# Kernel optimization log

Measured on AMD Instinct MI355X. Metric: run time of the kernel, lower is better.

## Reference

```python
import jax, jax.numpy as jnp
import numpy as np
from jax import lax

WIN_SIZE = 11
SIGMA = 1.5
K1, K2 = 0.01, 0.03
DATA_RANGE = 1.0


def _gauss_1d(size=WIN_SIZE, sigma=SIGMA):
    coords = jnp.arange(size, dtype=jnp.float32) - size // 2
    g = jnp.exp(-(coords ** 2) / (2.0 * sigma ** 2))
    return g / jnp.sum(g)


def _blur(x, win):
    # x: (1, C, H, W); separable depthwise gaussian, VALID padding (pytorch_msssim)
    C = x.shape[1]
    dn = ('NCHW', 'OIHW', 'NCHW')
    kw = jnp.tile(win.reshape(1, 1, 1, -1), (C, 1, 1, 1))  # (C,1,1,K)
    kh = jnp.tile(win.reshape(1, 1, -1, 1), (C, 1, 1, 1))  # (C,1,K,1)
    x = lax.conv_general_dilated(x, kw, (1, 1), 'VALID',
                                 dimension_numbers=dn, feature_group_count=C)
    x = lax.conv_general_dilated(x, kh, (1, 1), 'VALID',
                                 dimension_numbers=dn, feature_group_count=C)
    return x


def _ssim_loss(pred, targ, height, width):
    x = pred.reshape(1, 3, height, width)
    y = targ.reshape(1, 3, height, width)
    win = _gauss_1d()
    C1 = (K1 * DATA_RANGE) ** 2
    C2 = (K2 * DATA_RANGE) ** 2

    mu1 = _blur(x, win)
    mu2 = _blur(y, win)
    mu1_sq = mu1 * mu1
    mu2_sq = mu2 * mu2
    mu1_mu2 = mu1 * mu2
    sigma1_sq = _blur(x * x, win) - mu1_sq
    sigma2_sq = _blur(y * y, win) - mu2_sq
    sigma12 = _blur(x * y, win) - mu1_mu2

    cs_map = (2.0 * sigma12 + C2) / (sigma1_sq + sigma2_sq + C2)
    ssim_map = ((2.0 * mu1_mu2 + C1) / (mu1_sq + mu2_sq + C1)) * cs_map
    return 1.0 - jnp.mean(ssim_map)


def setup_inputs() -> dict:
    key = jax.random.key(0)
    k1, k2 = jax.random.split(key)
    H, W = 2048, 2048
    return {
        'predicted_img': jax.random.uniform(k1, (1, 3, H, W), dtype=jnp.float32),
        'target_img': jax.random.uniform(k2, (1, 3, H, W), dtype=jnp.float32),
        'height': H,
        'width': W,
    }


def reference(predicted_img, target_img, height, width):
    return _ssim_loss(predicted_img, target_img, height, width)
```

## Files before the change

### kernel.cpp

```cpp
#include <hip/hip_runtime.h>
#include <math.h>

typedef float f32x2 __attribute__((ext_vector_type(2)));
typedef float f32x4 __attribute__((ext_vector_type(4)));

#define HH    2048
#define WW    2048
#define NCH   3
#define NOUT  2038
#define OWID  64
#define OH    128
#define CROWS 8
#define BUF   20
#define HAW   66
#define HCW   68
#define NTX   32
#define NTY   16
#define NBLOCKS (NTX*NTY*NCH)
#define NOUT_TOTAL 12460332.0f

__device__ __forceinline__ float ssim_term(float mu1, float mu2,
                                           float b11, float b22, float b12) {
    const float c1v = 1e-4f, c2v = 9e-4f;
    float mu1sq = mu1 * mu1;
    float mu2sq = mu2 * mu2;
    float mu12  = mu1 * mu2;
    float s11 = b11 - mu1sq;
    float s22 = b22 - mu2sq;
    float s12 = b12 - mu12;
    float csn = 2.f * s12 + c2v;
    float csd = s11 + s22 + c2v;
    float ln  = 2.f * mu12 + c1v;
    float ld  = mu1sq + mu2sq + c1v;
    return (csn * ln) * __builtin_amdgcn_rcpf(csd * ld);
}

__global__ __launch_bounds__(256, 2)
void ssim_main(const float* __restrict__ x, const float* __restrict__ y,
               float* __restrict__ partials) {
    __shared__ f32x2 hbA[BUF][HAW];
    __shared__ f32x2 hbB[BUF][HAW];
    __shared__ float hbC[BUF][HCW];
    __shared__ float wsum[4];

    const int tid = threadIdx.x;
    const int gx0 = blockIdx.x * OWID;
    const int gy0 = blockIdx.y * OH;
    const float* xb = x + (size_t)blockIdx.z * HH * WW;
    const float* yb = y + (size_t)blockIdx.z * HH * WW;

    float w[11];
    {
        float s = 0.f;
        #pragma unroll
        for (int i = 0; i < 11; ++i) {
            float d = (float)(i - 5);
            w[i] = expf(-d * d / 4.5f);
            s += w[i];
        }
        float inv = 1.f / s;
        #pragma unroll
        for (int i = 0; i < 11; ++i) w[i] *= inv;
    }

    const int lr  = tid >> 5;
    const int c0  = (tid & 31) * 2;
    const int gxc = gx0 + c0;

    f32x4 px[3], py[3];

    auto PF = [&](int base) {
        int gy = gy0 + base + lr; if (gy > HH - 1) gy = HH - 1;
        const float* xr = xb + (size_t)gy * WW;
        const float* yr = yb + (size_t)gy * WW;
        #pragma unroll
        for (int a = 0; a < 3; ++a) {
            int g = gxc + 4 * a;
            if (g + 4 <= WW) {
                px[a] = *(const f32x4*)(xr + g);
                py[a] = *(const f32x4*)(yr + g);
            } else {
                int g0 = g     < WW ? g     : WW - 1;
                int g1 = g + 1 < WW ? g + 1 : WW - 1;
                int g2 = g + 2 < WW ? g + 2 : WW - 1;
                int g3 = g + 3 < WW ? g + 3 : WW - 1;
                px[a] = (f32x4){xr[g0], xr[g1], xr[g2], xr[g3]};
                py[a] = (f32x4){yr[g0], yr[g1], yr[g2], yr[g3]};
            }
        }
    };

    auto BLUR = [&](int base, bool tailMask) {
        int slot = (base + lr) % BUF;
        f32x2 p[12];
        #pragma unroll
        for (int a = 0; a < 3; ++a)
            #pragma unroll
            for (int i = 0; i < 4; ++i)
                p[4 * a + i] = (f32x2){px[a][i], py[a][i]};
        f32x2 q[12]; float pr[12];
        #pragma unroll
        for (int t = 0; t < 12; ++t) {
            q[t]  = p[t] * p[t];
            pr[t] = p[t].x * p[t].y;
        }
        f32x2 hA[2] = {}, hB[2] = {};
        float hC[2] = {};
        #pragma unroll
        for (int k = 0; k < 11; ++k) {
            f32x2 wk2 = (f32x2){w[k], w[k]};
            #pragma unroll
            for (int j = 0; j < 2; ++j) {
                hA[j] = __builtin_elementwise_fma(wk2, p[j + k], hA[j]);
                hB[j] = __builtin_elementwise_fma(wk2, q[j + k], hB[j]);
                hC[j] = fmaf(w[k], pr[j + k], hC[j]);
            }
        }
        if (!tailMask || lr < 2) {
            *(f32x4*)&hbA[slot][c0] = (f32x4){hA[0].x, hA[0].y, hA[1].x, hA[1].y};
            *(f32x4*)&hbB[slot][c0] = (f32x4){hB[0].x, hB[0].y, hB[1].x, hB[1].y};
            *(f32x2*)&hbC[slot][c0] = (f32x2){hC[0], hC[1]};
        }
    };

    float partial = 0.f;

    PF(0);  BLUR(0, false);
    PF(8);  BLUR(8, false);
    PF(16); BLUR(16, true);
    __syncthreads();

    const int col  = tid & 63;
    const int wid  = tid >> 6;
    const int ocol = gx0 + col;

    for (int m = 0; m < 16; ++m) {
        if (m < 15) PF(8 * m + 18);
        {
            const int r0 = 8 * m + wid * 2;
            int s = r0 % BUF;
            f32x2 aA[2] = {}, aB[2] = {};
            float aC[2] = {};
            #pragma unroll
            for (int j = 0; j < 12; ++j) {
                f32x2 va = hbA[s][col];
                f32x2 vb = hbB[s][col];
                float vc = hbC[s][col];
                #pragma unroll
                for (int i = 0; i < 2; ++i) {
                    const int k = j - i;
                    if (k >= 0 && k < 11) {
                        f32x2 wk2 = (f32x2){w[k], w[k]};
                        aA[i] = __builtin_elementwise_fma(wk2, va, aA[i]);
                        aB[i] = __builtin_elementwise_fma(wk2, vb, aB[i]);
                        aC[i] = fmaf(w[k], vc, aC[i]);
                    }
                }
                s = (s == BUF - 1) ? 0 : s + 1;
            }
            #pragma unroll
            for (int i = 0; i < 2; ++i) {
                int orow = gy0 + r0 + i;
                if (orow < NOUT && ocol < NOUT)
                    partial += ssim_term(aA[i].x, aA[i].y, aB[i].x, aB[i].y, aC[i]);
            }
        }
        __syncthreads();
        if (m < 15) {
            BLUR(8 * m + 18, false);
            __syncthreads();
        }
    }

    #pragma unroll
    for (int off = 32; off > 0; off >>= 1)
        partial += __shfl_down(partial, off, 64);
    if ((tid & 63) == 0) wsum[tid >> 6] = partial;
    __syncthreads();
    if (tid == 0) {
        int bid = (blockIdx.z * gridDim.y + blockIdx.y) * gridDim.x + blockIdx.x;
        partials[bid] = wsum[0] + wsum[1] + wsum[2] + wsum[3];
    }
}

__global__ __launch_bounds__(256)
void ssim_finalize(const float* __restrict__ partials, float* __restrict__ out) {
    __shared__ float ws[4];
    float s = 0.f;
    for (int i = threadIdx.x; i < NBLOCKS / 4; i += 256) {
        float4 v = ((const float4*)partials)[i];
        s += (v.x + v.y) + (v.z + v.w);
    }
    #pragma unroll
    for (int off = 32; off > 0; off >>= 1)
        s += __shfl_down(s, off, 64);
    if ((threadIdx.x & 63) == 0) ws[threadIdx.x >> 6] = s;
    __syncthreads();
    if (threadIdx.x == 0)
        out[0] = 1.f - (ws[0] + ws[1] + ws[2] + ws[3]) / NOUT_TOTAL;
}

extern "C" void kernel_launch(void* const* d_in, const int* in_sizes, int n_in,
                              void* d_out, int out_size, void* d_ws, size_t ws_size,
                              hipStream_t stream) {
    const float* x = (const float*)d_in[0];
    const float* y = (const float*)d_in[1];
    float* out = (float*)d_out;
    float* partials = (float*)d_ws;

    dim3 grid(NTX, NTY, NCH);
    ssim_main<<<grid, dim3(256), 0, stream>>>(x, y, partials);
    ssim_finalize<<<1, 256, 0, stream>>>(partials, out);
}
```

Before: 189.3 us.

## Stream rows per column-thread with register rotating vertical blur accumulators

Replaces the tiled two-pass shared-memory scheme with a streaming design. Each thread owns one output column and walks down a 45-row segment. The horizontal blur uses a small per-wave double-buffered LDS stage, and the vertical blur goes into 11 rotating register accumulators. This removes block-wide barriers and the large LDS ring buffer. In exchange it recomputes 10 halo rows per segment, uses many more registers, and issues scalar 4-byte global loads instead of vector loads.

```diff
diff --git a/kernel.cpp b/kernel.cpp
--- a/kernel.cpp
+++ b/kernel.cpp
@@ -2,21 +2,15 @@
 #include <math.h>
 
 typedef float f32x2 __attribute__((ext_vector_type(2)));
-typedef float f32x4 __attribute__((ext_vector_type(4)));
 
 #define HH    2048
 #define WW    2048
 #define NCH   3
 #define NOUT  2038
-#define OWID  64
-#define OH    128
-#define CROWS 8
-#define BUF   20
-#define HAW   66
-#define HCW   68
-#define NTX   32
-#define NTY   16
-#define NBLOCKS (NTX*NTY*NCH)
+#define SH    45
+#define NSEG  46
+#define NBX   8
+#define NBLOCKS (NBX*NSEG*NCH)
 #define NOUT_TOTAL 12460332.0f
 
 __device__ __forceinline__ float ssim_term(float mu1, float mu2,
@@ -38,138 +32,117 @@
 __global__ __launch_bounds__(256, 2)
 void ssim_main(const float* __restrict__ x, const float* __restrict__ y,
                float* __restrict__ partials) {
-    __shared__ f32x2 hbA[BUF][HAW];
-    __shared__ f32x2 hbB[BUF][HAW];
-    __shared__ float hbC[BUF][HCW];
+    __shared__ f32x2 stage[2][4][80];
     __shared__ float wsum[4];
 
-    const int tid = threadIdx.x;
-    const int gx0 = blockIdx.x * OWID;
-    const int gy0 = blockIdx.y * OH;
+    const int tid  = threadIdx.x;
+    const int lane = tid & 63;
+    const int wid  = tid >> 6;
+    const int col  = blockIdx.x * 256 + tid;
+    const int r0   = blockIdx.y * SH;
     const float* xb = x + (size_t)blockIdx.z * HH * WW;
     const float* yb = y + (size_t)blockIdx.z * HH * WW;
 
-    float w[11];
+    f32x2 w2[11];
     {
+        float wtmp[11];
         float s = 0.f;
         #pragma unroll
         for (int i = 0; i < 11; ++i) {
             float d = (float)(i - 5);
-            w[i] = expf(-d * d / 4.5f);
-            s += w[i];
+            wtmp[i] = expf(-d * d / 4.5f);
+            s += wtmp[i];
         }
         float inv = 1.f / s;
         #pragma unroll
-        for (int i = 0; i < 11; ++i) w[i] *= inv;
+        for (int i = 0; i < 11; ++i) w2[i] = (f32x2){wtmp[i] * inv, wtmp[i] * inv};
     }
 
-    const int lr  = tid >> 5;
-    const int c0  = (tid & 31) * 2;
-    const int gxc = gx0 + c0;
+    const int  cB    = (col + 64 < HH) ? col + 64 : HH - 1;
+    const bool colok = col < NOUT;
+    const bool tail  = lane < 16;
 
-    f32x4 px[3], py[3];
-
-    auto PF = [&](int base) {
-        int gy = gy0 + base + lr; if (gy > HH - 1) gy = HH - 1;
-        const float* xr = xb + (size_t)gy * WW;
-        const float* yr = yb + (size_t)gy * WW;
-        #pragma unroll
-        for (int a = 0; a < 3; ++a) {
-            int g = gxc + 4 * a;
-            if (g + 4 <= WW) {
-                px[a] = *(const f32x4*)(xr + g);
-                py[a] = *(const f32x4*)(yr + g);
-            } else {
-                int g0 = g     < WW ? g     : WW - 1;
-                int g1 = g + 1 < WW ? g + 1 : WW - 1;
-                int g2 = g + 2 < WW ? g + 2 : WW - 1;
-                int g3 = g + 3 < WW ? g + 3 : WW - 1;
-                px[a] = (f32x4){xr[g0], xr[g1], xr[g2], xr[g3]};
-                py[a] = (f32x4){yr[g0], yr[g1], yr[g2], yr[g3]};
-            }
-        }
-    };
-
-    auto BLUR = [&](int base, bool tailMask) {
-        int slot = (base + lr) % BUF;
-        f32x2 p[12];
-        #pragma unroll
-        for (int a = 0; a < 3; ++a)
-            #pragma unroll
-            for (int i = 0; i < 4; ++i)
-                p[4 * a + i] = (f32x2){px[a][i], py[a][i]};
-        f32x2 q[12]; float pr[12];
-        #pragma unroll
-        for (int t = 0; t < 12; ++t) {
-            q[t]  = p[t] * p[t];
-            pr[t] = p[t].x * p[t].y;
-        }
-        f32x2 hA[2] = {}, hB[2] = {};
-        float hC[2] = {};
-        #pragma unroll
-        for (int k = 0; k < 11; ++k) {
-            f32x2 wk2 = (f32x2){w[k], w[k]};
-            #pragma unroll
-            for (int j = 0; j < 2; ++j) {
-                hA[j] = __builtin_elementwise_fma(wk2, p[j + k], hA[j]);
-                hB[j] = __builtin_elementwise_fma(wk2, q[j + k], hB[j]);
-                hC[j] = fmaf(w[k], pr[j + k], hC[j]);
-            }
-        }
-        if (!tailMask || lr < 2) {
-            *(f32x4*)&hbA[slot][c0] = (f32x4){hA[0].x, hA[0].y, hA[1].x, hA[1].y};
-            *(f32x4*)&hbB[slot][c0] = (f32x4){hB[0].x, hB[0].y, hB[1].x, hB[1].y};
-            *(f32x2*)&hbC[slot][c0] = (f32x2){hC[0], hC[1]};
-        }
-    };
+    f32x2 accA[11], accB[11];
+    float accC[11];
+    #pragma unroll
+    for (int i = 0; i < 11; ++i) {
+        accA[i] = (f32x2){0.f, 0.f};
+        accB[i] = (f32x2){0.f, 0.f};
+        accC[i] = 0.f;
+    }
 
     float partial = 0.f;
 
-    PF(0);  BLUR(0, false);
-    PF(8);  BLUR(8, false);
-    PF(16); BLUR(16, true);
-    __syncthreads();
+    float cx0, cy0, cx1, cy1;
+    {
+        const float* xr = xb + (size_t)r0 * WW;
+        const float* yr = yb + (size_t)r0 * WW;
+        cx0 = xr[col]; cy0 = yr[col];
+        cx1 = xr[cB];  cy1 = yr[cB];
+    }
 
-    const int col  = tid & 63;
-    const int wid  = tid >> 6;
-    const int ocol = gx0 + col;
+#define PHASE(VB, PH, EMIT) do {                                               \
+    const int vrow = (VB) + (PH);                                              \
+    \
+    int nrow = r0 + vrow + 1; nrow = nrow < HH ? nrow : HH - 1;                \
+    const float* xr = xb + (size_t)nrow * WW;                                  \
+    const float* yr = yb + (size_t)nrow * WW;                                  \
+    float nx0 = xr[col], ny0 = yr[col];                                        \
+    float nx1 = xr[cB],  ny1 = yr[cB];                                         \
+             \
+    f32x2* sb = &stage[vrow & 1][wid][0];                                      \
+    sb[lane] = (f32x2){cx0, cy0};                                              \
+    if (tail) sb[64 + lane] = (f32x2){cx1, cy1};                               \
+            \
+    f32x2 p[11];                                                               \
+    _Pragma("unroll")                                                          \
+    for (int j = 0; j < 11; ++j) p[j] = sb[lane + j];                          \
+                                    \
+    f32x2 hA = w2[0] * p[0];                                                   \
+    f32x2 hB = w2[0] * (p[0] * p[0]);                                          \
+    float hC = w2[0].x * (p[0].x * p[0].y);                                    \
+    _Pragma("unroll")                                                          \
+    for (int k = 1; k < 11; ++k) {                                             \
+        hA = __builtin_elementwise_fma(w2[k], p[k], hA);                       \
+        hB = __builtin_elementwise_fma(w2[k], p[k] * p[k], hB);                \
+        hC = fmaf(w2[k].x, p[k].x * p[k].y, hC);                               \
+    }                                                                          \
+     \
+     \
+     \
+    accA[(PH)] = w2[0] * hA;                                                   \
+    accB[(PH)] = w2[0] * hB;                                                   \
+    accC[(PH)] = w2[0].x * hC;                                                 \
+    _Pragma("unroll")                                                          \
+    for (int k = 1; k < 11; ++k) {                                             \
+        const int sidx = ((PH) + 11 - k) % 11;                                 \
+        accA[sidx] = __builtin_elementwise_fma(w2[k], hA, accA[sidx]);         \
+        accB[sidx] = __builtin_elementwise_fma(w2[k], hB, accB[sidx]);         \
+        accC[sidx] = fmaf(w2[k].x, hC, accC[sidx]);                            \
+    }                                                                          \
+     \
+    if (EMIT) {                                                                \
+        const int e = ((PH) + 1) % 11;                                         \
+        const int orow = r0 + vrow - 10;                                       \
+        if (orow < NOUT && colok)                                              \
+            partial += ssim_term(accA[e].x, accA[e].y,                         \
+                                 accB[e].x, accB[e].y, accC[e]);               \
+    }                                                                          \
+    cx0 = nx0; cy0 = ny0; cx1 = nx1; cy1 = ny1;                                \
+} while (0)
 
-    for (int m = 0; m < 16; ++m) {
-        if (m < 15) PF(8 * m + 18);
-        {
-            const int r0 = 8 * m + wid * 2;
-            int s = r0 % BUF;
-            f32x2 aA[2] = {}, aB[2] = {};
-            float aC[2] = {};
-            #pragma unroll
-            for (int j = 0; j < 12; ++j) {
-                f32x2 va = hbA[s][col];
-                f32x2 vb = hbB[s][col];
-                float vc = hbC[s][col];
-                #pragma unroll
-                for (int i = 0; i < 2; ++i) {
-                    const int k = j - i;
-                    if (k >= 0 && k < 11) {
-                        f32x2 wk2 = (f32x2){w[k], w[k]};
-                        aA[i] = __builtin_elementwise_fma(wk2, va, aA[i]);
-                        aB[i] = __builtin_elementwise_fma(wk2, vb, aB[i]);
-                        aC[i] = fmaf(w[k], vc, aC[i]);
-                    }
-                }
-                s = (s == BUF - 1) ? 0 : s + 1;
-            }
-            #pragma unroll
-            for (int i = 0; i < 2; ++i) {
-                int orow = gy0 + r0 + i;
-                if (orow < NOUT && ocol < NOUT)
-                    partial += ssim_term(aA[i].x, aA[i].y, aB[i].x, aB[i].y, aC[i]);
-            }
-        }
-        __syncthreads();
-        if (m < 15) {
-            BLUR(8 * m + 18, false);
-            __syncthreads();
-        }
+    PHASE(0, 0, false); PHASE(0, 1, false); PHASE(0, 2, false);
+    PHASE(0, 3, false); PHASE(0, 4, false); PHASE(0, 5, false);
+    PHASE(0, 6, false); PHASE(0, 7, false); PHASE(0, 8, false);
+    PHASE(0, 9, false); PHASE(0, 10, true);
+
+    #pragma unroll 1
+    for (int it = 1; it < 5; ++it) {
+        const int vb = it * 11;
+        PHASE(vb, 0, true);  PHASE(vb, 1, true);  PHASE(vb, 2, true);
+        PHASE(vb, 3, true);  PHASE(vb, 4, true);  PHASE(vb, 5, true);
+        PHASE(vb, 6, true);  PHASE(vb, 7, true);  PHASE(vb, 8, true);
+        PHASE(vb, 9, true);  PHASE(vb, 10, true);
     }
 
     #pragma unroll
@@ -208,7 +181,7 @@
     float* out = (float*)d_out;
     float* partials = (float*)d_ws;
 
-    dim3 grid(NTX, NTY, NCH);
+    dim3 grid(NBX, NSEG, NCH);
     ssim_main<<<grid, dim3(256), 0, stream>>>(x, y, partials);
     ssim_finalize<<<1, 256, 0, stream>>>(partials, out);
 }
```

Result: faster. 171.0 us (-9.7%).
